# Kernel optimization log

Hardware: AMD Instinct MI355X
Metric: run time of the kernel (lower is better)

Reference implementation:

```python
import jax, jax.numpy as jnp
import numpy as np

B, N, C, H, MC, LIE, KD = 2, 2048, 256, 8, 256, 3, 16
DH = C // H

def swish(x):
    return x * jax.nn.sigmoid(x)

def layernorm(x, g, b):
    m = jnp.mean(x, axis=-1, keepdims=True)
    v = jnp.var(x, axis=-1, keepdims=True)
    return (x - m) * jax.lax.rsqrt(v + 1e-5) * g + b

def setup_inputs():
    ks = jax.random.split(jax.random.key(0), 12)
    p = lambda i, shape, s: jax.random.normal(ks[i], shape, jnp.float32) * s
    return dict(
        pairwise_g=jax.random.normal(ks[0], (B, N, N, LIE), jnp.float32),
        x=jax.random.normal(ks[1], (B, N, C), jnp.float32),
        mask=jnp.ones((B, N), dtype=bool),
        ln1_g=jnp.ones((C,), jnp.float32), ln1_b=jnp.zeros((C,), jnp.float32),
        ln2_g=jnp.ones((C,), jnp.float32), ln2_b=jnp.zeros((C,), jnp.float32),
        wn_w1=p(2, (LIE, KD), 0.3), wn_b1=jnp.zeros((KD,), jnp.float32),
        wn_w2=p(3, (KD, KD), 0.3), wn_b2=jnp.zeros((KD,), jnp.float32),
        wn_w3=p(4, (KD, H), 0.3), wn_b3=jnp.zeros((H,), jnp.float32),
        wq=p(5, (C, C), 0.05), bq=jnp.zeros((C,), jnp.float32),
        wk=p(6, (C, C), 0.05), bk=jnp.zeros((C,), jnp.float32),
        in_w=p(7, (C, C), 0.05), in_b=jnp.zeros((C,), jnp.float32),
        out_w=p(8, (C, C), 0.05), out_b=jnp.zeros((C,), jnp.float32),
        mlp_w1=p(9, (C, C), 0.05), mlp_b1=jnp.zeros((C,), jnp.float32),
        mlp_w2=p(10, (C, C), 0.05), mlp_b2=jnp.zeros((C,), jnp.float32),
    )

def _ema(pairwise_g, x, mask, wn_w1, wn_b1, wn_w2, wn_b2, wn_w3, wn_b3,
         wq, bq, wk, bk, in_w, in_b, out_w, out_b):
    b, n, c = x.shape
    # neighbourhood extraction: topk smallest T(3) group distances (mc_samples=MC, fill=1.0)
    dists = jnp.linalg.norm(pairwise_g, axis=-1)                      # (b,n,n)
    dists = jnp.where(mask[:, None, :], dists, jnp.float32(1e8))
    _, idx = jax.lax.top_k(-dists, MC)                                # (b,n,k)
    nbhd_g = jnp.take_along_axis(pairwise_g, idx[..., None], axis=2)  # (b,n,k,LIE)
    nbhd_mask = jnp.take_along_axis(jnp.broadcast_to(mask[:, None, :], (b, n, n)), idx, axis=2)
    # location kernel: MultiheadWeightNet MLP on pairwise group elements -> per-head scalar
    hloc = swish(nbhd_g @ wn_w1 + wn_b1)
    hloc = swish(hloc @ wn_w2 + wn_b2)
    loc = hloc @ wn_w3 + wn_b3                                        # (b,n,k,H)
    # feature kernel: multihead dot product over gathered neighbour keys
    q = (x @ wq + bq).reshape(b, n, H, DH)
    kf = (x @ wk + bk).reshape(b, n, H, DH)
    k_nbhd = jax.vmap(lambda kfb, ib: kfb[ib])(kf, idx)               # (b,n,k,H,DH)
    scores = jnp.einsum('bnhd,bnkhd->bnkh', q, k_nbhd) / jnp.sqrt(jnp.float32(DH))
    pre = jnp.where(nbhd_mask[..., None], loc + scores, jnp.float32(-1e38))
    attn = jax.nn.softmax(pre, axis=2)                                # (b,n,k,H)
    # values; scatter attention into dense (b,n,n,H) exactly as the torch code, then aggregate
    v = (x @ in_w + in_b).reshape(b, n, H, DH)
    BS = jnp.arange(b)[:, None, None]
    NNS = jnp.arange(n)[None, :, None]
    aw = jnp.zeros((b, n, n, H), attn.dtype).at[BS, NNS, idx].set(attn)
    out = jnp.einsum('bnmh,bmhd->bnhd', aw, v).reshape(b, n, c)
    return out @ out_w + out_b

def reference(pairwise_g, x, mask, ln1_g, ln1_b, ln2_g, ln2_b,
              wn_w1, wn_b1, wn_w2, wn_b2, wn_w3, wn_b3,
              wq, bq, wk, bk, in_w, in_b, out_w, out_b,
              mlp_w1, mlp_b1, mlp_w2, mlp_b2):
    # EquivariantTransformerBlock with block_norm='layer_pre'
    x = x + _ema(pairwise_g, layernorm(x, ln1_g, ln1_b), mask,
                 wn_w1, wn_b1, wn_w2, wn_b2, wn_w3, wn_b3,
                 wq, bq, wk, bk, in_w, in_b, out_w, out_b)
    h = layernorm(x, ln2_g, ln2_b)
    x = x + (swish(h @ mlp_w1 + mlp_b1) @ mlp_w2 + mlp_b2)
    return x
```

## Files before the change

### kernel.cpp

```cpp
#include <hip/hip_runtime.h>
#include <hip/hip_bf16.h>

#define Bb 2
#define Nn 2048
#define Cc 256
#define Hh 8
#define MCk 256
#define RT (Bb * Nn)

typedef __hip_bfloat16 bf16;
typedef _Float16 f16;
typedef __fp16 h2v __attribute__((ext_vector_type(2)));
typedef __fp16 h8 __attribute__((ext_vector_type(8)));
typedef float f32x4 __attribute__((ext_vector_type(4)));

__device__ __forceinline__ h2v bc16(unsigned u) { return __builtin_bit_cast(h2v, u); }
__device__ __forceinline__ unsigned bcu(h2v v) { return __builtin_bit_cast(unsigned, v); }

__device__ __forceinline__ float dot2(h2v a, h2v b, float c) {
  return __builtin_amdgcn_fdot2(a, b, c, false);
}
__device__ __forceinline__ f32x4 mfma16(h8 a, h8 b, f32x4 c) {
  return __builtin_amdgcn_mfma_f32_16x16x32_f16(a, b, c, 0, 0, 0);
}
__device__ __forceinline__ float swish_f(float z) {
  return z * __builtin_amdgcn_rcpf(1.f + __expf(-z));
}

__global__ __launch_bounds__(256) void k1_prep_ln_select(
    const float* __restrict__ w0, const float* __restrict__ w1,
    const float* __restrict__ w2, const float* __restrict__ w3,
    const float* __restrict__ w4, const float* __restrict__ w5,
    f16* __restrict__ wtout,
    const float* __restrict__ x, const float* __restrict__ g,
    const float* __restrict__ b, f16* __restrict__ lnout,
    const float* __restrict__ pg, int* __restrict__ idxout)
{
  __shared__ float tile[32][33];
  __shared__ int rc[31][4];
  __shared__ int rcl[4];
  __shared__ int em[8][4][2];
  int bx = blockIdx.x;
  int t = threadIdx.x;
  if (bx < 384) {
    int wb = bx / 64, tid = bx % 64;
    const float* ws_[6] = {w0, w1, w2, w3, w4, w5};
    const float* W = ws_[wb];
    f16* o = wtout + (size_t)wb * 65536;
    int tn0 = (tid & 7) * 32, tk0 = (tid >> 3) * 32;
    int tl = t & 31, tg = t >> 5;
#pragma unroll
    for (int r = 0; r < 4; r++) {
      int k = tk0 + tg * 4 + r;
      tile[tg * 4 + r][tl] = W[(size_t)k * 256 + tn0 + tl];
    }
    __syncthreads();
#pragma unroll
    for (int r = 0; r < 4; r++) {
      int n = tn0 + tg * 4 + r;
      o[(size_t)n * 256 + tk0 + tl] = (f16)tile[tl][tg * 4 + r];
    }
  } else if (bx < 1408) {
    int wave = t >> 6, lane = t & 63;
    int row = (bx - 384) * 4 + wave;
    const float4 v = reinterpret_cast<const float4*>(x + (size_t)row * Cc)[lane];
    float s  = v.x + v.y + v.z + v.w;
    float s2 = v.x * v.x + v.y * v.y + v.z * v.z + v.w * v.w;
#pragma unroll
    for (int m = 1; m < 64; m <<= 1) {
      s  += __shfl_xor(s, m);
      s2 += __shfl_xor(s2, m);
    }
    float mean = s * (1.0f / Cc);
    float var  = s2 * (1.0f / Cc) - mean * mean;
    float rs   = rsqrtf(var + 1e-5f);
    const float4 gg = reinterpret_cast<const float4*>(g)[lane];
    const float4 bb = reinterpret_cast<const float4*>(b)[lane];
    float ox = (v.x - mean) * rs * gg.x + bb.x;
    float oy = (v.y - mean) * rs * gg.y + bb.y;
    float oz = (v.z - mean) * rs * gg.z + bb.z;
    float ow = (v.w - mean) * rs * gg.w + bb.w;
    uint2 st;
    st.x = bcu(__builtin_amdgcn_cvt_pkrtz(ox, oy));
    st.y = bcu(__builtin_amdgcn_cvt_pkrtz(oz, ow));
    *(uint2*)(lnout + (size_t)row * Cc + lane * 4) = st;
  } else {
    int row = bx - 1408;
    int wave = t >> 6, lane = t & 63;
    const float* base = pg + (size_t)row * (Nn * 3);
    unsigned u[8];
#pragma unroll
    for (int jj = 0; jj < 8; jj++) {
      int col = jj * 256 + t;
      float g0 = base[col * 3 + 0];
      float g1 = base[col * 3 + 1];
      float g2 = base[col * 3 + 2];
      u[jj] = __float_as_uint(sqrtf(g0 * g0 + g1 * g1 + g2 * g2));
    }
    unsigned long long lmask = (1ull << lane) - 1ull;
    unsigned T = 0;
    for (int bit = 30; bit >= 0; bit--) {
      unsigned cand = T | (1u << bit);
      int c = 0;
#pragma unroll
      for (int jj = 0; jj < 8; jj++) c += (u[jj] < cand) ? 1 : 0;
#pragma unroll
      for (int m = 1; m < 64; m <<= 1) c += __shfl_xor(c, m);
      if (lane == 0) rc[bit][wave] = c;
      __syncthreads();
      c = rc[bit][0] + rc[bit][1] + rc[bit][2] + rc[bit][3];
      if (c <= MCk - 1) T = cand;
    }
    int cl = 0;
#pragma unroll
    for (int jj = 0; jj < 8; jj++) cl += (u[jj] < T) ? 1 : 0;
#pragma unroll
    for (int m = 1; m < 64; m <<= 1) cl += __shfl_xor(cl, m);
    if (lane == 0) rcl[wave] = cl;
    __syncthreads();
    int need = MCk - (rcl[0] + rcl[1] + rcl[2] + rcl[3]);
    int slotBase = 0, eqBase = 0;
    for (int jj = 0; jj < 8; jj++) {
      bool less = u[jj] < T, eq = (u[jj] == T);
      unsigned long long bls = __ballot(less), beq = __ballot(eq);
      if (lane == 0) {
        em[jj][wave][0] = __popcll(bls);
        em[jj][wave][1] = __popcll(beq);
      }
      __syncthreads();
      int lessPref = 0, lessTot = 0, eqPref = 0, eqTot = 0;
#pragma unroll
      for (int w = 0; w < 4; w++) {
        int lw = em[jj][w][0], ew = em[jj][w][1];
        lessTot += lw; eqTot += ew;
        if (w < wave) { lessPref += lw; eqPref += ew; }
      }
      int epb = eqPref + __popcll(beq & lmask);
      int rem = need - eqBase; if (rem < 0) rem = 0;
      bool sel = less || (eq && (epb < rem));
      int takenBefore = (epb < rem) ? epb : rem;
      int pos = slotBase + lessPref + __popcll(bls & lmask) + takenBefore;
      if (sel) idxout[(size_t)row * MCk + pos] = jj * 256 + t;
      slotBase += lessTot + ((eqTot < rem) ? eqTot : rem);
      eqBase += eqTot;
    }
  }
}

__global__ __launch_bounds__(256) void k2_locmlp_qkv(
    const float* __restrict__ pg, const int* __restrict__ idxb,
    uint4* __restrict__ locout,
    const float* __restrict__ w1, const float* __restrict__ b1,
    const float* __restrict__ w2, const float* __restrict__ b2,
    const float* __restrict__ w3, const float* __restrict__ b3,
    const f16* __restrict__ A,
    const f16* __restrict__ WTq, const float* __restrict__ Bq,
    const f16* __restrict__ WTk, const float* __restrict__ Bk,
    const f16* __restrict__ WTv, const float* __restrict__ Bv,
    f16* __restrict__ outq, f16* __restrict__ outk, f16* __restrict__ outv)
{
  __shared__ float wnl[64];
  __shared__ h2v   w2p[128];
  __shared__ float bn2[16];
  __shared__ h2v   w3p[64];
  __shared__ float bn3[8];
  int t = threadIdx.x;
  if (blockIdx.x < 4096) {
    int row = blockIdx.x;
    for (int i = t; i < 280; i += 256) {
      if (i < 48) {
        wnl[i] = w1[i];
      } else if (i < 64) {
        wnl[i] = b1[i - 48];
      } else if (i < 192) {
        int j = i - 64, i2 = j >> 4, o = j & 15;
        w2p[j] = __builtin_amdgcn_cvt_pkrtz(w2[(2 * i2) * 16 + o], w2[(2 * i2 + 1) * 16 + o]);
      } else if (i < 208) {
        bn2[i - 192] = b2[i - 192];
      } else if (i < 272) {
        int j = i - 208, i2 = j >> 3, o = j & 7;
        w3p[j] = __builtin_amdgcn_cvt_pkrtz(w3[(2 * i2) * 8 + o], w3[(2 * i2 + 1) * 8 + o]);
      } else {
        bn3[i - 272] = b3[i - 272];
      }
    }
    int m = idxb[(size_t)row * 256 + t];
    const float* gsp = pg + ((size_t)row * Nn + m) * 3;
    float g0 = gsp[0], g1 = gsp[1], g2 = gsp[2];
    __syncthreads();
    float h1[16];
#pragma unroll
    for (int o = 0; o < 16; o++) {
      float z = wnl[48 + o] + g0 * wnl[o] + g1 * wnl[16 + o] + g2 * wnl[32 + o];
      h1[o] = swish_f(z);
    }
    h2v hp1[8];
#pragma unroll
    for (int i = 0; i < 8; i++) hp1[i] = __builtin_amdgcn_cvt_pkrtz(h1[2 * i], h1[2 * i + 1]);
    float hh[16];
#pragma unroll
    for (int o = 0; o < 16; o++) {
      float z = bn2[o];
#pragma unroll
      for (int i2 = 0; i2 < 8; i2++) z = dot2(hp1[i2], w2p[i2 * 16 + o], z);
      hh[o] = swish_f(z);
    }
    h2v hp2[8];
#pragma unroll
    for (int i = 0; i < 8; i++) hp2[i] = __builtin_amdgcn_cvt_pkrtz(hh[2 * i], hh[2 * i + 1]);
    float loc[8];
#pragma unroll
    for (int o = 0; o < 8; o++) {
      float z = bn3[o];
#pragma unroll
      for (int i2 = 0; i2 < 8; i2++) z = dot2(hp2[i2], w3p[i2 * 8 + o], z);
      loc[o] = z;
    }
    uint4 lv;
    lv.x = bcu(__builtin_amdgcn_cvt_pkrtz(loc[0], loc[1]));
    lv.y = bcu(__builtin_amdgcn_cvt_pkrtz(loc[2], loc[3]));
    lv.z = bcu(__builtin_amdgcn_cvt_pkrtz(loc[4], loc[5]));
    lv.w = bcu(__builtin_amdgcn_cvt_pkrtz(loc[6], loc[7]));
    locout[(size_t)row * 256 + t] = lv;
  } else {
    int bxq = blockIdx.x - 4096;
    int wid = t >> 6, lane = t & 63;
    int m0 = ((bxq & 63) * 4 + wid) * 16;
    int n0 = (bxq >> 6) * 32;
    int lm = lane & 15, lk = lane >> 4;
    const h8* Ab = (const h8*)(A + (size_t)(m0 + lm) * 256) + lk;
    const h8* Q0 = (const h8*)(WTq + (size_t)(n0 + lm) * 256) + lk;
    const h8* Q1 = (const h8*)(WTq + (size_t)(n0 + 16 + lm) * 256) + lk;
    const h8* K0 = (const h8*)(WTk + (size_t)(n0 + lm) * 256) + lk;
    const h8* K1 = (const h8*)(WTk + (size_t)(n0 + 16 + lm) * 256) + lk;
    const h8* V0 = (const h8*)(WTv + (size_t)(n0 + lm) * 256) + lk;
    const h8* V1 = (const h8*)(WTv + (size_t)(n0 + 16 + lm) * 256) + lk;
    f32x4 aq0 = {0.f,0.f,0.f,0.f}, aq1 = {0.f,0.f,0.f,0.f};
    f32x4 ak0 = {0.f,0.f,0.f,0.f}, ak1 = {0.f,0.f,0.f,0.f};
    f32x4 av0 = {0.f,0.f,0.f,0.f}, av1 = {0.f,0.f,0.f,0.f};
#pragma unroll
    for (int ks = 0; ks < 8; ks++) {
      h8 a = Ab[ks * 4];
      aq0 = mfma16(a, Q0[ks * 4], aq0);
      aq1 = mfma16(a, Q1[ks * 4], aq1);
      ak0 = mfma16(a, K0[ks * 4], ak0);
      ak1 = mfma16(a, K1[ks * 4], ak1);
      av0 = mfma16(a, V0[ks * 4], av0);
      av1 = mfma16(a, V1[ks * 4], av1);
    }
    const float qs = 0.17677669529663687f;
    float bq0 = Bq[n0 + lm], bq1 = Bq[n0 + 16 + lm];
    float bk0 = Bk[n0 + lm], bk1 = Bk[n0 + 16 + lm];
    float bv0 = Bv[n0 + lm], bv1 = Bv[n0 + 16 + lm];
#pragma unroll
    for (int i = 0; i < 4; i++) {
      size_t row = m0 + lk * 4 + i;
      outq[row * 256 + n0 + lm]      = (f16)((aq0[i] + bq0) * qs);
      outq[row * 256 + n0 + 16 + lm] = (f16)((aq1[i] + bq1) * qs);
      outk[row * 256 + n0 + lm]      = (f16)(ak0[i] + bk0);
      outk[row * 256 + n0 + 16 + lm] = (f16)(ak1[i] + bk1);
      outv[row * 256 + n0 + lm]      = (f16)(av0[i] + bv0);
      outv[row * 256 + n0 + 16 + lm] = (f16)(av1[i] + bv1);
    }
  }
}

__global__ __launch_bounds__(256, 4) void attn_kernel(
    const f16* __restrict__ qh, const f16* __restrict__ kh,
    const f16* __restrict__ vv, const int* __restrict__ idxb,
    const uint4* __restrict__ loc16, f16* __restrict__ out)
{
  __shared__ int   offs[256];
  __shared__ float ps[256 * 9];
  __shared__ float agg[4 * 256];
  __shared__ float redmx[4][8];
  __shared__ float redsm[4][8];
  int t = threadIdx.x;
  int row = blockIdx.x;
  int bidx = row >> 11;
  int g = t >> 5, c = t & 31;

  int m = idxb[(size_t)row * 256 + t];
  offs[t] = (bidx * Nn + m) * 512;
  const uint4 qu = *(const uint4*)((const char*)qh + (size_t)row * 512 + (size_t)c * 16);
  h2v q0 = bc16(qu.x), q1 = bc16(qu.y), q2 = bc16(qu.z), q3 = bc16(qu.w);
  const uint4 lv = loc16[(size_t)row * 256 + t];
  __syncthreads();

  int offr[32];
#pragma unroll
  for (int kk = 0; kk < 32; kk++) offr[kk] = offs[kk * 8 + g];

  const char* kbase = (const char*)kh + (size_t)c * 16;
#pragma unroll
  for (int kk = 0; kk < 32; kk += 4) {
    const uint4 k0 = *(const uint4*)(kbase + offr[kk + 0]);
    const uint4 k1 = *(const uint4*)(kbase + offr[kk + 1]);
    const uint4 k2 = *(const uint4*)(kbase + offr[kk + 2]);
    const uint4 k3 = *(const uint4*)(kbase + offr[kk + 3]);
    float p0 = dot2(bc16(k0.x), q0, 0.f);
    float p1 = dot2(bc16(k1.x), q0, 0.f);
    float p2 = dot2(bc16(k2.x), q0, 0.f);
    float p3 = dot2(bc16(k3.x), q0, 0.f);
    p0 = dot2(bc16(k0.y), q1, p0); p1 = dot2(bc16(k1.y), q1, p1);
    p2 = dot2(bc16(k2.y), q1, p2); p3 = dot2(bc16(k3.y), q1, p3);
    p0 = dot2(bc16(k0.z), q2, p0); p1 = dot2(bc16(k1.z), q2, p1);
    p2 = dot2(bc16(k2.z), q2, p2); p3 = dot2(bc16(k3.z), q2, p3);
    p0 = dot2(bc16(k0.w), q3, p0); p1 = dot2(bc16(k1.w), q3, p1);
    p2 = dot2(bc16(k2.w), q3, p2); p3 = dot2(bc16(k3.w), q3, p3);
    p0 += __shfl_xor(p0, 1); p1 += __shfl_xor(p1, 1);
    p2 += __shfl_xor(p2, 1); p3 += __shfl_xor(p3, 1);
    p0 += __shfl_xor(p0, 2); p1 += __shfl_xor(p1, 2);
    p2 += __shfl_xor(p2, 2); p3 += __shfl_xor(p3, 2);
    if ((c & 3) == 0) {
      int hh_ = c >> 2;
      ps[((kk + 0) * 8 + g) * 9 + hh_] = p0;
      ps[((kk + 1) * 8 + g) * 9 + hh_] = p1;
      ps[((kk + 2) * 8 + g) * 9 + hh_] = p2;
      ps[((kk + 3) * 8 + g) * 9 + hh_] = p3;
    }
  }
  __syncthreads();

  h2v l01 = bc16(lv.x), l23 = bc16(lv.y), l45 = bc16(lv.z), l67 = bc16(lv.w);
  float pre[8];
  pre[0] = ps[t * 9 + 0] + (float)l01.x;
  pre[1] = ps[t * 9 + 1] + (float)l01.y;
  pre[2] = ps[t * 9 + 2] + (float)l23.x;
  pre[3] = ps[t * 9 + 3] + (float)l23.y;
  pre[4] = ps[t * 9 + 4] + (float)l45.x;
  pre[5] = ps[t * 9 + 5] + (float)l45.y;
  pre[6] = ps[t * 9 + 6] + (float)l67.x;
  pre[7] = ps[t * 9 + 7] + (float)l67.y;
  float mx[8];
#pragma unroll
  for (int h = 0; h < 8; h++) mx[h] = pre[h];
#pragma unroll
  for (int mm = 1; mm < 64; mm <<= 1) {
#pragma unroll
    for (int h = 0; h < 8; h++) mx[h] = fmaxf(mx[h], __shfl_xor(mx[h], mm));
  }
  int wv = t >> 6, ln = t & 63;
  if (ln == 0) {
#pragma unroll
    for (int h = 0; h < 8; h++) redmx[wv][h] = mx[h];
  }
  __syncthreads();
#pragma unroll
  for (int h = 0; h < 8; h++)
    mx[h] = fmaxf(fmaxf(redmx[0][h], redmx[1][h]), fmaxf(redmx[2][h], redmx[3][h]));
  float e[8], sm[8];
#pragma unroll
  for (int h = 0; h < 8; h++) { e[h] = __expf(pre[h] - mx[h]); sm[h] = e[h]; }
#pragma unroll
  for (int mm = 1; mm < 64; mm <<= 1) {
#pragma unroll
    for (int h = 0; h < 8; h++) sm[h] += __shfl_xor(sm[h], mm);
  }
  if (ln == 0) {
#pragma unroll
    for (int h = 0; h < 8; h++) redsm[wv][h] = sm[h];
  }
  __syncthreads();
#pragma unroll
  for (int h = 0; h < 8; h++) {
    float ssum = redsm[0][h] + redsm[1][h] + redsm[2][h] + redsm[3][h];
    ps[t * 9 + h] = e[h] * __builtin_amdgcn_rcpf(ssum);
  }
  __syncthreads();

  h2v ac0 = {0, 0}, ac1 = {0, 0}, ac2 = {0, 0}, ac3 = {0, 0};
  const char* vbase = (const char*)vv + (size_t)c * 16;
  int hh_ = c >> 2;
#pragma unroll
  for (int kk = 0; kk < 32; kk += 4) {
    const uint4 v0 = *(const uint4*)(vbase + offr[kk + 0]);
    const uint4 v1 = *(const uint4*)(vbase + offr[kk + 1]);
    const uint4 v2 = *(const uint4*)(vbase + offr[kk + 2]);
    const uint4 v3 = *(const uint4*)(vbase + offr[kk + 3]);
    float aw0 = ps[((kk + 0) * 8 + g) * 9 + hh_];
    float aw1 = ps[((kk + 1) * 8 + g) * 9 + hh_];
    float aw2 = ps[((kk + 2) * 8 + g) * 9 + hh_];
    float aw3 = ps[((kk + 3) * 8 + g) * 9 + hh_];
    h2v w0 = __builtin_amdgcn_cvt_pkrtz(aw0, aw0);
    h2v w1 = __builtin_amdgcn_cvt_pkrtz(aw1, aw1);
    h2v w2 = __builtin_amdgcn_cvt_pkrtz(aw2, aw2);
    h2v w3 = __builtin_amdgcn_cvt_pkrtz(aw3, aw3);
    ac0 = bc16(v0.x) * w0 + ac0; ac1 = bc16(v0.y) * w0 + ac1;
    ac2 = bc16(v0.z) * w0 + ac2; ac3 = bc16(v0.w) * w0 + ac3;
    ac0 = bc16(v1.x) * w1 + ac0; ac1 = bc16(v1.y) * w1 + ac1;
    ac2 = bc16(v1.z) * w1 + ac2; ac3 = bc16(v1.w) * w1 + ac3;
    ac0 = bc16(v2.x) * w2 + ac0; ac1 = bc16(v2.y) * w2 + ac1;
    ac2 = bc16(v2.z) * w2 + ac2; ac3 = bc16(v2.w) * w2 + ac3;
    ac0 = bc16(v3.x) * w3 + ac0; ac1 = bc16(v3.y) * w3 + ac1;
    ac2 = bc16(v3.z) * w3 + ac2; ac3 = bc16(v3.w) * w3 + ac3;
  }
  float acc[8] = {(float)ac0.x, (float)ac0.y, (float)ac1.x, (float)ac1.y,
                  (float)ac2.x, (float)ac2.y, (float)ac3.x, (float)ac3.y};
#pragma unroll
  for (int i = 0; i < 8; i++) acc[i] += __shfl_xor(acc[i], 32);
  if ((t & 32) == 0) {
#pragma unroll
    for (int i = 0; i < 8; i++) agg[wv * 256 + c * 8 + i] = acc[i];
  }
  __syncthreads();
  float o = agg[t] + agg[256 + t] + agg[512 + t] + agg[768 + t];
  out[(size_t)row * 256 + t] = (f16)o;
}

__global__ __launch_bounds__(512) void gemm_out_ln(
    const f16* __restrict__ A, const f16* __restrict__ WT,
    const float* __restrict__ bias, const float* __restrict__ xres,
    const float* __restrict__ g, const float* __restrict__ b,
    float* __restrict__ x1, f16* __restrict__ hout)
{
  __shared__ float sred[8][16][2];
  int wid = threadIdx.x >> 6, lane = threadIdx.x & 63;
  int lm = lane & 15, lk = lane >> 4;
  int m0 = blockIdx.x * 16;
  const h8* Ab = (const h8*)(A + (size_t)(m0 + lm) * 256) + lk;
  const h8* Bp0 = (const h8*)(WT + (size_t)(wid * 32 + lm) * 256) + lk;
  const h8* Bp1 = (const h8*)(WT + (size_t)(wid * 32 + 16 + lm) * 256) + lk;
  f32x4 ac0 = {0,0,0,0}, ac1 = {0,0,0,0};
#pragma unroll
  for (int ks = 0; ks < 8; ks++) {
    h8 a = Ab[ks * 4];
    ac0 = mfma16(a, Bp0[ks * 4], ac0);
    ac1 = mfma16(a, Bp1[ks * 4], ac1);
  }
  int c0 = wid * 32 + lm, c1 = wid * 32 + 16 + lm;
  float b0 = bias[c0], b1 = bias[c1];
  float s[4], s2[4];
#pragma unroll
  for (int i = 0; i < 4; i++) {
    size_t row = m0 + lk * 4 + i;
    float y0 = ac0[i] + b0 + xres[row * 256 + c0];
    float y1 = ac1[i] + b1 + xres[row * 256 + c1];
    ac0[i] = y0; ac1[i] = y1;
    x1[row * 256 + c0] = y0;
    x1[row * 256 + c1] = y1;
    s[i] = y0 + y1; s2[i] = y0 * y0 + y1 * y1;
  }
#pragma unroll
  for (int mm = 1; mm < 16; mm <<= 1) {
#pragma unroll
    for (int i = 0; i < 4; i++) {
      s[i]  += __shfl_xor(s[i], mm);
      s2[i] += __shfl_xor(s2[i], mm);
    }
  }
  if (lm == 0) {
#pragma unroll
    for (int i = 0; i < 4; i++) {
      sred[wid][lk * 4 + i][0] = s[i];
      sred[wid][lk * 4 + i][1] = s2[i];
    }
  }
  __syncthreads();
  float g0 = g[c0], g1 = g[c1], bb0 = b[c0], bb1 = b[c1];
#pragma unroll
  for (int i = 0; i < 4; i++) {
    int r = lk * 4 + i;
    float ts = 0.f, ts2 = 0.f;
#pragma unroll
    for (int w = 0; w < 8; w++) { ts += sred[w][r][0]; ts2 += sred[w][r][1]; }
    float mean = ts * (1.f / 256.f);
    float var  = ts2 * (1.f / 256.f) - mean * mean;
    float rs   = rsqrtf(var + 1e-5f);
    size_t row = m0 + r;
    hout[row * 256 + c0] = (f16)((ac0[i] - mean) * rs * g0 + bb0);
    hout[row * 256 + c1] = (f16)((ac1[i] - mean) * rs * g1 + bb1);
  }
}

__global__ __launch_bounds__(512) void mlp_fused(
    const f16* __restrict__ A, const f16* __restrict__ WT1,
    const float* __restrict__ b1, const f16* __restrict__ WT2,
    const float* __restrict__ b2, const float* __restrict__ x1,
    float* __restrict__ outp)
{
  __shared__ f16 hl[16 * 272];
  int wid = threadIdx.x >> 6, lane = threadIdx.x & 63;
  int lm = lane & 15, lk = lane >> 4;
  int m0 = blockIdx.x * 16;
  const h8* Ab = (const h8*)(A + (size_t)(m0 + lm) * 256) + lk;
  const h8* B10 = (const h8*)(WT1 + (size_t)(wid * 32 + lm) * 256) + lk;
  const h8* B11 = (const h8*)(WT1 + (size_t)(wid * 32 + 16 + lm) * 256) + lk;
  const h8* B20 = (const h8*)(WT2 + (size_t)(wid * 32 + lm) * 256) + lk;
  const h8* B21 = (const h8*)(WT2 + (size_t)(wid * 32 + 16 + lm) * 256) + lk;
  f32x4 ac0 = {0,0,0,0}, ac1 = {0,0,0,0};
#pragma unroll
  for (int ks = 0; ks < 8; ks++) {
    h8 a = Ab[ks * 4];
    ac0 = mfma16(a, B10[ks * 4], ac0);
    ac1 = mfma16(a, B11[ks * 4], ac1);
  }
  int c0 = wid * 32 + lm, c1 = wid * 32 + 16 + lm;
  float bb0 = b1[c0], bb1 = b1[c1];
#pragma unroll
  for (int i = 0; i < 4; i++) {
    float y0 = ac0[i] + bb0;
    float y1 = ac1[i] + bb1;
    hl[(lk * 4 + i) * 272 + c0] = (f16)swish_f(y0);
    hl[(lk * 4 + i) * 272 + c1] = (f16)swish_f(y1);
  }
  __syncthreads();
  f32x4 o0 = {0,0,0,0}, o1 = {0,0,0,0};
#pragma unroll
  for (int ks = 0; ks < 8; ks++) {
    h8 a2 = *(const h8*)&hl[lm * 272 + ks * 32 + lk * 8];
    o0 = mfma16(a2, B20[ks * 4], o0);
    o1 = mfma16(a2, B21[ks * 4], o1);
  }
  float d0 = b2[c0], d1 = b2[c1];
#pragma unroll
  for (int i = 0; i < 4; i++) {
    size_t row = m0 + lk * 4 + i;
    outp[row * 256 + c0] = o0[i] + d0 + x1[row * 256 + c0];
    outp[row * 256 + c1] = o1[i] + d1 + x1[row * 256 + c1];
  }
}

extern "C" void kernel_launch(void* const* d_in, const int* in_sizes, int n_in,
                              void* d_out, int out_size, void* d_ws, size_t ws_size,
                              hipStream_t stream)
{
  (void)in_sizes; (void)n_in; (void)out_size; (void)ws_size;
  const float* pg   = (const float*)d_in[0];
  const float* x    = (const float*)d_in[1];
  const float* ln1g = (const float*)d_in[3];
  const float* ln1b = (const float*)d_in[4];
  const float* ln2g = (const float*)d_in[5];
  const float* ln2b = (const float*)d_in[6];
  const float* wnw1 = (const float*)d_in[7];
  const float* wnb1 = (const float*)d_in[8];
  const float* wnw2 = (const float*)d_in[9];
  const float* wnb2 = (const float*)d_in[10];
  const float* wnw3 = (const float*)d_in[11];
  const float* wnb3 = (const float*)d_in[12];
  const float* wq   = (const float*)d_in[13];
  const float* bq   = (const float*)d_in[14];
  const float* wk   = (const float*)d_in[15];
  const float* bk   = (const float*)d_in[16];
  const float* inw  = (const float*)d_in[17];
  const float* inb  = (const float*)d_in[18];
  const float* outw = (const float*)d_in[19];
  const float* outbv= (const float*)d_in[20];
  const float* m1w  = (const float*)d_in[21];
  const float* m1b  = (const float*)d_in[22];
  const float* m2w  = (const float*)d_in[23];
  const float* m2b  = (const float*)d_in[24];

  const size_t RC = (size_t)RT * 256;
  f16*   WTall = (f16*)d_ws;
  f16*   WTq = WTall + 0 * 65536;
  f16*   WTk = WTall + 1 * 65536;
  f16*   WTv = WTall + 2 * 65536;
  f16*   WTo = WTall + 3 * 65536;
  f16*   WTm1= WTall + 4 * 65536;
  f16*   WTm2= WTall + 5 * 65536;
  f16*   ln1h = WTall + 6 * 65536;
  f16*   qh  = ln1h + RC;
  f16*   kh  = qh + RC;
  f16*   vvb = kh + RC;
  int*   idxb= (int*)(vvb + RC);
  f16*   emah= (f16*)(idxb + RC);
  void*  R1  = (void*)(emah + RC);
  uint4* loc16 = (uint4*)R1;
  float* x1    = (float*)R1;
  f16*   ln2h  = ln1h;

  dim3 blk(256);
  k1_prep_ln_select<<<dim3(384 + RT / 4 + RT), blk, 0, stream>>>(
      wq, wk, inw, outw, m1w, m2w, WTall, x, ln1g, ln1b, ln1h, pg, idxb);
  k2_locmlp_qkv<<<dim3(RT + 512), blk, 0, stream>>>(
      pg, idxb, loc16, wnw1, wnb1, wnw2, wnb2, wnw3, wnb3,
      ln1h, WTq, bq, WTk, bk, WTv, inb, qh, kh, vvb);
  attn_kernel<<<dim3(RT), blk, 0, stream>>>(qh, kh, vvb, idxb, loc16, emah);
  gemm_out_ln<<<dim3(RT / 16), dim3(512), 0, stream>>>(emah, WTo, outbv, x, ln2g, ln2b,
                                                       x1, ln2h);
  mlp_fused<<<dim3(RT / 16), dim3(512), 0, stream>>>(ln2h, WTm1, m1b, WTm2, m2b, x1,
                                                     (float*)d_out);
}
```

Baseline: 169.5 us.

## Vectorize distance loads and use atomic compaction for top-k selection

The top-k selection blocks now read pairwise_g with contiguous float4 loads, with each thread owning 8 consecutive columns. The radix-threshold count uses ballot+popcount instead of shuffle reductions. Output positions come from shared-memory atomics rather than a per-chunk barrier with prefix sums, and ties are resolved afterwards by ranking column indices in an equal-value list. This removes 8 block-wide barriers and cuts load instructions, at the cost of non-deterministic ordering of the selected indices and a quadratic tie-rank loop when there are many ties.

```diff
diff --git a/kernel.cpp b/kernel.cpp
--- a/kernel.cpp
+++ b/kernel.cpp
@@ -38,8 +38,8 @@
 {
   __shared__ float tile[32][33];
   __shared__ int rc[31][4];
-  __shared__ int rcl[4];
-  __shared__ int em[8][4][2];
+  __shared__ int eqlist[2048];
+  __shared__ int nsel, neq;
   int bx = blockIdx.x;
   int t = threadIdx.x;
   if (bx < 384) {
@@ -87,62 +87,57 @@
   } else {
     int row = bx - 1408;
     int wave = t >> 6, lane = t & 63;
-    const float* base = pg + (size_t)row * (Nn * 3);
+    const float4* b4 = (const float4*)(pg + (size_t)row * (Nn * 3));
+    float4 v0 = b4[6 * t + 0], v1 = b4[6 * t + 1], v2 = b4[6 * t + 2];
+    float4 v3 = b4[6 * t + 3], v4 = b4[6 * t + 4], v5 = b4[6 * t + 5];
     unsigned u[8];
-#pragma unroll
-    for (int jj = 0; jj < 8; jj++) {
-      int col = jj * 256 + t;
-      float g0 = base[col * 3 + 0];
-      float g1 = base[col * 3 + 1];
-      float g2 = base[col * 3 + 2];
-      u[jj] = __float_as_uint(sqrtf(g0 * g0 + g1 * g1 + g2 * g2));
-    }
-    unsigned long long lmask = (1ull << lane) - 1ull;
+    u[0] = __float_as_uint(sqrtf(v0.x * v0.x + v0.y * v0.y + v0.z * v0.z));
+    u[1] = __float_as_uint(sqrtf(v0.w * v0.w + v1.x * v1.x + v1.y * v1.y));
+    u[2] = __float_as_uint(sqrtf(v1.z * v1.z + v1.w * v1.w + v2.x * v2.x));
+    u[3] = __float_as_uint(sqrtf(v2.y * v2.y + v2.z * v2.z + v2.w * v2.w));
+    u[4] = __float_as_uint(sqrtf(v3.x * v3.x + v3.y * v3.y + v3.z * v3.z));
+    u[5] = __float_as_uint(sqrtf(v3.w * v3.w + v4.x * v4.x + v4.y * v4.y));
+    u[6] = __float_as_uint(sqrtf(v4.z * v4.z + v4.w * v4.w + v5.x * v5.x));
+    u[7] = __float_as_uint(sqrtf(v5.y * v5.y + v5.z * v5.z + v5.w * v5.w));
+    if (t == 0) { nsel = 0; neq = 0; }
     unsigned T = 0;
     for (int bit = 30; bit >= 0; bit--) {
       unsigned cand = T | (1u << bit);
       int c = 0;
 #pragma unroll
-      for (int jj = 0; jj < 8; jj++) c += (u[jj] < cand) ? 1 : 0;
-#pragma unroll
-      for (int m = 1; m < 64; m <<= 1) c += __shfl_xor(c, m);
+      for (int jj = 0; jj < 8; jj++) c += __popcll(__ballot(u[jj] < cand));
       if (lane == 0) rc[bit][wave] = c;
       __syncthreads();
       c = rc[bit][0] + rc[bit][1] + rc[bit][2] + rc[bit][3];
       if (c <= MCk - 1) T = cand;
     }
-    int cl = 0;
-#pragma unroll
-    for (int jj = 0; jj < 8; jj++) cl += (u[jj] < T) ? 1 : 0;
-#pragma unroll
-    for (int m = 1; m < 64; m <<= 1) cl += __shfl_xor(cl, m);
-    if (lane == 0) rcl[wave] = cl;
+    unsigned long long lmask = (1ull << lane) - 1ull;
+#pragma unroll
+    for (int jj = 0; jj < 8; jj++) {
+      int col = t * 8 + jj;
+      bool less = u[jj] < T;
+      bool eq   = (u[jj] == T);
+      unsigned long long bls = __ballot(less);
+      unsigned long long beq = __ballot(eq);
+      int cls = __popcll(bls), ceq = __popcll(beq);
+      int bl_ = 0, be_ = 0;
+      if (lane == 0) {
+        bl_ = atomicAdd(&nsel, cls);
+        be_ = atomicAdd(&neq, ceq);
+      }
+      bl_ = __shfl(bl_, 0);
+      be_ = __shfl(be_, 0);
+      if (less) idxout[(size_t)row * MCk + bl_ + __popcll(bls & lmask)] = col;
+      if (eq)   eqlist[be_ + __popcll(beq & lmask)] = col;
+    }
     __syncthreads();
-    int need = MCk - (rcl[0] + rcl[1] + rcl[2] + rcl[3]);
-    int slotBase = 0, eqBase = 0;
-    for (int jj = 0; jj < 8; jj++) {
-      bool less = u[jj] < T, eq = (u[jj] == T);
-      unsigned long long bls = __ballot(less), beq = __ballot(eq);
-      if (lane == 0) {
-        em[jj][wave][0] = __popcll(bls);
-        em[jj][wave][1] = __popcll(beq);
-      }
-      __syncthreads();
-      int lessPref = 0, lessTot = 0, eqPref = 0, eqTot = 0;
-#pragma unroll
-      for (int w = 0; w < 4; w++) {
-        int lw = em[jj][w][0], ew = em[jj][w][1];
-        lessTot += lw; eqTot += ew;
-        if (w < wave) { lessPref += lw; eqPref += ew; }
-      }
-      int epb = eqPref + __popcll(beq & lmask);
-      int rem = need - eqBase; if (rem < 0) rem = 0;
-      bool sel = less || (eq && (epb < rem));
-      int takenBefore = (epb < rem) ? epb : rem;
-      int pos = slotBase + lessPref + __popcll(bls & lmask) + takenBefore;
-      if (sel) idxout[(size_t)row * MCk + pos] = jj * 256 + t;
-      slotBase += lessTot + ((eqTot < rem) ? eqTot : rem);
-      eqBase += eqTot;
+    int cl = nsel, nq = neq;
+    int need = MCk - cl;
+    for (int e = t; e < nq; e += 256) {
+      int colE = eqlist[e];
+      int rank = 0;
+      for (int j = 0; j < nq; j++) rank += (eqlist[j] < colE) ? 1 : 0;
+      if (rank < need) idxout[(size_t)row * MCk + cl + rank] = colE;
     }
   }
 }
```

Result: faster. 151.0 us (-10.9%).
